# Kernel optimization log

Hardware: AMD Instinct MI355X
Metric: run time of the kernel (lower is better)

## Reference

```python
import jax, jax.numpy as jnp
import numpy as np

B, L, H, D = 2, 1024, 8, 64
DIM = H * D


def setup_inputs() -> dict:
    key = jax.random.key(0)
    ks = jax.random.split(key, 12)
    s = 0.02  # weight init scale
    return {
        "x": jax.random.normal(ks[0], (B, L, DIM), dtype=jnp.float32),
        "wq_w": jax.random.normal(ks[1], (DIM, DIM), dtype=jnp.float32) * s,
        "wq_b": jax.random.normal(ks[2], (DIM,), dtype=jnp.float32) * s,
        "wk_w": jax.random.normal(ks[3], (DIM, DIM), dtype=jnp.float32) * s,
        "wk_b": jax.random.normal(ks[4], (DIM,), dtype=jnp.float32) * s,
        "wv_w": jax.random.normal(ks[5], (DIM, DIM), dtype=jnp.float32) * s,
        "wv_b": jax.random.normal(ks[6], (DIM,), dtype=jnp.float32) * s,
        "phazor_re": jax.random.normal(ks[7], (H, D), dtype=jnp.float32),
        "phazor_im": jax.random.normal(ks[8], (H, D), dtype=jnp.float32),
        "amplitude": jax.random.normal(ks[9], (H,), dtype=jnp.float32),
        "last_conv_re": jax.random.normal(ks[10], (H, D, D), dtype=jnp.float32),
        "last_conv_im": jax.random.normal(ks[11], (H, D, D), dtype=jnp.float32),
    }


def reference(x, wq_w, wq_b, wk_w, wk_b, wv_w, wv_b,
              phazor_re, phazor_im, amplitude, last_conv_re, last_conv_im):
    b, l, _ = x.shape
    h, d = phazor_re.shape
    cplx = jnp.complex64

    q = (x @ wq_w.T + wq_b).reshape(b, l, h, d)
    k = (x @ wk_w.T + wk_b).reshape(b, l, h, d)
    v = (x @ wv_w.T + wv_b).reshape(b, l, h, d)

    phazor_p = (phazor_re + 1j * phazor_im).astype(cplx)      # (H,D)
    phase = phazor_p / jnp.abs(phazor_p)                      # unit-modulus
    amp = jax.nn.sigmoid(amplitude)                           # (H,)
    phazor = phase * amp[:, None]                             # (H,D)

    t = jnp.arange(l)
    phase_prog = phase[None] ** t[:, None, None]              # (L,H,D)
    phase_prog_inv = phase[None] ** (-t)[:, None, None]       # (L,H,D)
    phazor_prog = phazor[None] ** t[:, None, None]            # (L,H,D)

    # cross-chunk: q_t * phazor^{t+1} contracted with initial state (detached)
    last_conv = (last_conv_re + 1j * last_conv_im).astype(cplx)  # (H,D,D)
    qc = q.astype(cplx) * (phazor_prog * phazor[None])[None]     # (B,L,H,D)
    cross = jnp.einsum('blhd,hde->blhe', qc, last_conv)          # (B,L,H,D)

    # decay mask: amp^(i-j) on the lower triangle
    diff = t[:, None] - t[None, :]
    tril = diff >= 0
    mask = jnp.where(tril[None],
                     amp[:, None, None] ** jnp.where(tril, diff, 0)[None],
                     0.0)                                        # (H,L,L)

    qph = q.astype(cplx) * phase_prog[None]                      # (B,L,H,D)
    kph = k.astype(cplx) * phase_prog_inv[None]                  # (B,L,H,D)
    qk = jnp.einsum('blhd,bmhd->bhlm', qph, kph)                 # (B,H,L,L) complex
    qk_mask = qk * mask[None].astype(cplx)
    inner = jnp.einsum('bhlm,bmhd->blhd', qk_mask, v.astype(cplx))

    out = (inner + cross).real.astype(x.dtype).reshape(b, l, h * d)
    return out
```

## Files before the change

### kernel.cpp

```cpp
#include <hip/hip_runtime.h>
#include <hip/hip_bf16.h>
#include <math.h>

#define L_SEQ 1024
#define DIMSZ 512
#define NH 8
#define ND 64
#define NB 2
#define CHUNK 64
#define NC (L_SEQ / CHUNK)
#define BHTOT (NB * NH)
#define MTOT 2048
#define KEFF 512
#define BM 64
#define BN 128

typedef __attribute__((ext_vector_type(8))) _Float16 f16x8;
typedef __attribute__((ext_vector_type(4))) float f32x4;

#define GLD16(g, l) __builtin_amdgcn_global_load_lds( \
    (const __attribute__((address_space(1))) unsigned int*)(g), \
    (__attribute__((address_space(3))) unsigned int*)(l), 16, 0, 0)

__device__ static inline unsigned short f2h(float f) {
    union { _Float16 h; unsigned short u; } x;
    x.h = (_Float16)f;
    return x.u;
}
__device__ static inline float h2f(unsigned short u) {
    union { unsigned short u; _Float16 h; } x;
    x.u = u;
    return (float)x.h;
}
__device__ static inline unsigned packh2(float a, float b) {
    return (unsigned)f2h(a) | ((unsigned)f2h(b) << 16);
}

__global__ __launch_bounds__(256) void pack_kernel(
    const float* __restrict__ x,
    const float* __restrict__ wq, const float* __restrict__ wk, const float* __restrict__ wv,
    const float* __restrict__ lc_re, const float* __restrict__ lc_im,
    unsigned short* __restrict__ A, unsigned short* __restrict__ Bm,
    unsigned* __restrict__ lcT)
{
    __shared__ unsigned T[64][65];
    const int bid = blockIdx.x;
    const int tid = threadIdx.x;
    if (bid < 1024) {
        const int i = bid * 256 + tid;
        const int n  = i >> 7;
        const int kq = (i & 127) << 2;
        const float4 xv = *(const float4*)(x + (size_t)n * DIMSZ + kq);
        *(ushort4*)(A + (size_t)n * KEFF + kq) =
            make_ushort4(f2h(xv.x), f2h(xv.y), f2h(xv.z), f2h(xv.w));
    } else if (bid < 1792) {
        const int idx = bid - 1024;
        const int which = idx >> 8;
        const float* w = which == 0 ? wq : (which == 1 ? wk : wv);
        const int i = (idx & 255) * 256 + tid;
        const int o  = i >> 7;
        const int kq = (i & 127) << 2;
        const float4 wv4 = *(const float4*)(w + (size_t)o * DIMSZ + kq);
        const int row = (which == 0) ? o
                      : 512 + (which - 1) * 64 + (o >> 6) * 128 + (o & 63);
        *(ushort4*)(Bm + (size_t)row * KEFF + kq) =
            make_ushort4(f2h(wv4.x), f2h(wv4.y), f2h(wv4.z), f2h(wv4.w));
    } else {
        const int h = bid - 1792;
        const int e = tid & 63;
        #pragma unroll
        for (int i = 0; i < 16; ++i) {
            const int d = i*4 + (tid >> 6);
            T[e][d] = packh2(lc_re[h*4096 + d*64 + e], lc_im[h*4096 + d*64 + e]);
        }
        __syncthreads();
        const int d = tid & 63;
        #pragma unroll
        for (int i = 0; i < 16; ++i) {
            const int e2 = i*4 + (tid >> 6);
            lcT[h*4096 + e2*64 + d] = T[e2][d];
        }
    }
}

__global__ __launch_bounds__(256) void gemm_kv_kernel(
    const unsigned short* __restrict__ A, const unsigned short* __restrict__ Bm,
    const float* __restrict__ bq, const float* __restrict__ bk, const float* __restrict__ bv,
    const float* __restrict__ ph_re, const float* __restrict__ ph_im,
    const float* __restrict__ ampl,
    unsigned short* __restrict__ qo, unsigned short* __restrict__ ko,
    unsigned short* __restrict__ vo, unsigned* __restrict__ kvB)
{
    __shared__ __align__(16) char lds[49152];
    const int tid  = threadIdx.x;
    const int lane = tid & 63;
    const int wave = tid >> 6;

    const int bid0 = blockIdx.x;
    const int sw = (bid0 & 7) * 48 + (bid0 >> 3);
    const bool isQ = sw < 128;
    int mtile, brow0, h = 0, panel = 0;
    if (isQ) { panel = sw & 3; mtile = sw >> 2; brow0 = panel * 128; }
    else     { const int r = sw - 128; h = r & 7; mtile = r >> 3; brow0 = 512 + h * 128; }
    const int row0 = mtile * 64;
    const int wr = wave >> 1, wc = wave & 1;

    const int srow = tid >> 3;
    const int sin  = (tid & 7) << 4;
    size_t goffA[2], goffB[4];
    #pragma unroll
    for (int c = 0; c < 2; ++c) {
        const int row = c * 32 + srow;
        const int swz = sin ^ ((row & 7) << 4);
        goffA[c] = (size_t)(row0 + row) * (KEFF * 2) + swz;
    }
    #pragma unroll
    for (int c = 0; c < 4; ++c) {
        const int row = c * 32 + srow;
        const int swz = sin ^ ((row & 7) << 4);
        goffB[c] = (size_t)(brow0 + row) * (KEFF * 2) + swz;
    }
    const int ldst = tid * 16;
    const char* Abyte = (const char*)A;
    const char* Bbyte = (const char*)Bm;

    f32x4 acc[2][4];
    const f32x4 zf = {0.f, 0.f, 0.f, 0.f};
    #pragma unroll
    for (int m = 0; m < 2; ++m)
        #pragma unroll
        for (int n = 0; n < 4; ++n) acc[m][n] = zf;

    auto stage = [&](int buf, int t) {
        char* la = lds + buf * 24576;
        char* lb = la + 8192;
        const size_t kb = (size_t)t * 128;
        #pragma unroll
        for (int c = 0; c < 2; ++c)
            GLD16(Abyte + goffA[c] + kb, la + c * 4096 + ldst);
        #pragma unroll
        for (int c = 0; c < 4; ++c)
            GLD16(Bbyte + goffB[c] + kb, lb + c * 4096 + ldst);
    };

    const int rl = lane & 15;
    const int kg = lane >> 4;
    const int rswz = (rl & 7) << 4;

    auto compute = [&](int buf) {
        const char* la = lds + buf * 24576;
        const char* lb = la + 8192;
        #pragma unroll
        for (int ks = 0; ks < 2; ++ks) {
            f16x8 av[2], bvv[4];
            #pragma unroll
            for (int m = 0; m < 2; ++m) {
                const int row = wr * 32 + m * 16 + rl;
                const int addr = (row * 128 + ks * 64 + kg * 16) ^ rswz;
                av[m] = *(const f16x8*)(la + addr);
            }
            #pragma unroll
            for (int n = 0; n < 4; ++n) {
                const int row = wc * 64 + n * 16 + rl;
                const int addr = (row * 128 + ks * 64 + kg * 16) ^ rswz;
                bvv[n] = *(const f16x8*)(lb + addr);
            }
            #pragma unroll
            for (int m = 0; m < 2; ++m)
                #pragma unroll
                for (int n = 0; n < 4; ++n)
                    acc[m][n] = __builtin_amdgcn_mfma_f32_16x16x32_f16(
                        av[m], bvv[n], acc[m][n], 0, 0, 0);
        }
    };

    stage(0, 0);
    __syncthreads();
    const int NT = KEFF / 64;
    for (int t = 0; t < NT; ++t) {
        if (t + 1 < NT) stage((t + 1) & 1, t + 1);
        compute(t & 1);
        __syncthreads();
    }

    if (isQ) {
        #pragma unroll
        for (int n = 0; n < 4; ++n) {
            const int cabs = panel * 128 + wc * 64 + n * 16 + rl;
            const float bs = bq[cabs];
            #pragma unroll
            for (int m = 0; m < 2; ++m) {
                const int rb = row0 + wr * 32 + m * 16 + kg * 4;
                #pragma unroll
                for (int r = 0; r < 4; ++r)
                    qo[(size_t)(rb + r) * DIMSZ + cabs] = f2h(acc[m][n][r] + bs);
            }
        }
        return;
    }

    _Float16 (*KTR)[72] = (_Float16(*)[72])(lds);
    _Float16 (*KTI)[72] = (_Float16(*)[72])(lds + 9216);
    _Float16 (*VWT)[72] = (_Float16(*)[72])(lds + 18432);

    unsigned short* outp = wc == 0 ? ko : vo;
    _Float16 (*RAW)[72] = wc == 0 ? KTR : VWT;
    #pragma unroll
    for (int n = 0; n < 4; ++n) {
        const int cl = h * 64 + n * 16 + rl;
        const float bs = (wc == 0 ? bk : bv)[cl];
        #pragma unroll
        for (int m = 0; m < 2; ++m) {
            const int jb = wr * 32 + m * 16 + kg * 4;
            #pragma unroll
            for (int r = 0; r < 4; ++r) {
                const float val = acc[m][n][r] + bs;
                outp[(size_t)(row0 + jb + r) * DIMSZ + cl] = f2h(val);
                RAW[n * 16 + rl][jb + r] = (_Float16)val;
            }
        }
    }
    __syncthreads();

    const float amp = 1.0f / (1.0f + expf(-ampl[h]));
    const float la_ = logf(amp);
    const float th = atan2f(ph_im[h*ND + lane], ph_re[h*ND + lane]);
    float sth2, cth2; sincosf(th, &sth2, &cth2);
    const float p0 = (float)(CHUNK - 1 - (wave*16 + 15));
    float ap = expf(la_ * p0);
    float sp, cp; sincosf(th * p0, &sp, &cp);
    #pragma unroll
    for (int jj = 15; jj >= 0; --jj) {
        const int j = wave*16 + jj;
        const float kk = (float)KTR[lane][j];
        const float vv = (float)VWT[lane][j];
        KTR[lane][j] = (_Float16)(kk * cp);
        KTI[lane][j] = (_Float16)(kk * sp);
        VWT[lane][j] = (_Float16)(vv * ap);
        const float ncp = cp*cth2 - sp*sth2;
        sp = cp*sth2 + sp*cth2; cp = ncp;
        ap *= amp;
    }
    __syncthreads();

    const int b = mtile >> 4, c = mtile & 15;
    unsigned* dst = kvB + (size_t)(((b * NH + h) << 4) | c) * (ND * ND);
    #pragma unroll
    for (int i = 0; i < 4; ++i) {
        const int mt = wave, nt = i;
        f32x4 aR = zf, aI = zf;
        #pragma unroll
        for (int ks = 0; ks < 2; ++ks) {
            const f16x8 av = *(const f16x8*)&VWT[mt*16 + rl][ks*32 + kg*8];
            const f16x8 br = *(const f16x8*)&KTR[nt*16 + rl][ks*32 + kg*8];
            const f16x8 bi = *(const f16x8*)&KTI[nt*16 + rl][ks*32 + kg*8];
            aR = __builtin_amdgcn_mfma_f32_16x16x32_f16(av, br, aR, 0, 0, 0);
            aI = __builtin_amdgcn_mfma_f32_16x16x32_f16(av, bi, aI, 0, 0, 0);
        }
        const int d = nt*16 + rl;
        #pragma unroll
        for (int r = 0; r < 4; ++r) {
            const int e = mt*16 + kg*4 + r;
            dst[e*ND + d] = packh2(aR[r], aI[r]);
        }
    }
}

__global__ __launch_bounds__(256) void scan_kernel(
    unsigned* __restrict__ kvB, const unsigned* __restrict__ lcT,
    const float* __restrict__ ph_re, const float* __restrict__ ph_im,
    const float* __restrict__ ampl)
{
    const int gid = blockIdx.x * 256 + threadIdx.x;
    const int bh = gid >> 12;
    const int idx = gid & 4095;
    const int h = bh & 7;
    const int d = idx & 63;

    const float th = atan2f(ph_im[h*ND + d], ph_re[h*ND + d]);
    const float la = -logf(1.0f + expf(-ampl[h]));
    const float ampC = expf(la * (float)CHUNK);
    float s, ct; sincosf(th * (float)CHUNK, &s, &ct);
    const float aCr = ampC * ct, aCi = ampC * s;

    unsigned* base = kvB + (size_t)bh * NC * (ND*ND) + idx;
    unsigned tl[NC];
    #pragma unroll
    for (int cc = 0; cc < NC; ++cc) tl[cc] = base[(size_t)cc * (ND*ND)];

    const unsigned lcp = lcT[h*4096 + idx];
    float Sr = h2f((unsigned short)(lcp & 0xffffu));
    float Si = h2f((unsigned short)(lcp >> 16));
    #pragma unroll
    for (int cc = 0; cc < NC; ++cc) {
        base[(size_t)cc * (ND*ND)] = packh2(Sr, Si);
        const float tr = h2f((unsigned short)(tl[cc] & 0xffffu));
        const float ti = h2f((unsigned short)(tl[cc] >> 16));
        const float nr = aCr*Sr - aCi*Si + tr;
        const float ni = aCr*Si + aCi*Sr + ti;
        Sr = nr; Si = ni;
    }
}

__global__ __launch_bounds__(256) void chunk_out_kernel(
    const unsigned short* __restrict__ q, const unsigned short* __restrict__ k,
    const unsigned short* __restrict__ v, const unsigned* __restrict__ Bst,
    const float* __restrict__ ph_re, const float* __restrict__ ph_im,
    const float* __restrict__ ampl, float* __restrict__ out)
{
    __shared__ __align__(16) _Float16 QhR[32][72], QhI[32][72];
    __shared__ __align__(16) _Float16 KhR[64][72], KhI[64][72];
    __shared__ __align__(16) _Float16 VT[64][72];
    __shared__ __align__(16) _Float16 SA[32][72];
    __shared__ float apw[80];

    const int half = blockIdx.x & 1;
    const int bhc = blockIdx.x >> 1;
    const int c  = bhc & (NC - 1);
    const int bh = bhc >> 4;
    const int b = bh >> 3, h = bh & 7;
    const int tid = threadIdx.x;
    const int lane = tid & 63, w = tid >> 6;
    const int rl = lane & 15, kg = lane >> 4;
    const int mt = w >> 1;

    const float la = -logf(1.0f + expf(-ampl[h]));
    if (tid < 72) apw[tid] = expf(la * (float)tid);
    const float th = atan2f(ph_im[h*ND + lane], ph_re[h*ND + lane]);
    float sth_, cth_; sincosf(th, &sth_, &cth_);

    unsigned breg[16];
    const unsigned* Bb = Bst + (size_t)bhc * (ND*ND);
    #pragma unroll
    for (int ii = 0; ii < 16; ++ii) breg[ii] = Bb[ii*256 + tid];

    {
        const int jbase = half*32 + w*8;
        float sr, cr; sincosf(th * (float)jbase, &sr, &cr);
        #pragma unroll
        for (int jj = 0; jj < 8; ++jj) {
            const int row = w*8 + jj;
            const int jabs = jbase + jj;
            const size_t off = ((size_t)(b*L_SEQ + c*CHUNK + jabs)) * DIMSZ + h*ND + lane;
            const float qq = h2f(q[off]);
            QhR[row][lane] = (_Float16)(qq * cr);
            QhI[row][lane] = (_Float16)(qq * sr);
            const float ncr = cr*cth_ - sr*sth_;
            sr = cr*sth_ + sr*cth_; cr = ncr;
        }
    }
    {
        const int kbase = w*16;
        float skr, ckr; sincosf(th * (float)kbase, &skr, &ckr);
        #pragma unroll
        for (int jj = 0; jj < 16; ++jj) {
            const int j = kbase + jj;
            if (half == 0 && j >= 32) {
                VT[lane][j] = (_Float16)0.f;
            } else {
                const size_t off = ((size_t)(b*L_SEQ + c*CHUNK + j)) * DIMSZ + h*ND + lane;
                const float kk = h2f(k[off]), vv = h2f(v[off]);
                KhR[j][lane] = (_Float16)(kk * ckr);
                KhI[j][lane] = (_Float16)(kk * skr);
                VT[lane][j]  = (_Float16)vv;
            }
            const float nck = ckr*cth_ - skr*sth_;
            skr = ckr*sth_ + skr*cth_; ckr = nck;
        }
    }
    __syncthreads();

    const f32x4 zf = {0.f, 0.f, 0.f, 0.f};
    f32x4 sacc[2] = {zf, zf};
    #pragma unroll
    for (int t = 0; t < 2; ++t) {
        const int nt = (w & 1)*2 + t;
        #pragma unroll
        for (int ks = 0; ks < 2; ++ks) {
            const f16x8 aR = *(const f16x8*)&QhR[mt*16 + rl][ks*32 + kg*8];
            const f16x8 bR = *(const f16x8*)&KhR[nt*16 + rl][ks*32 + kg*8];
            sacc[t] = __builtin_amdgcn_mfma_f32_16x16x32_f16(aR, bR, sacc[t], 0, 0, 0);
            const f16x8 aI = *(const f16x8*)&QhI[mt*16 + rl][ks*32 + kg*8];
            const f16x8 bI = *(const f16x8*)&KhI[nt*16 + rl][ks*32 + kg*8];
            sacc[t] = __builtin_amdgcn_mfma_f32_16x16x32_f16(aI, bI, sacc[t], 0, 0, 0);
        }
    }
    __syncthreads();

    #pragma unroll
    for (int t = 0; t < 2; ++t) {
        const int nt = (w & 1)*2 + t;
        #pragma unroll
        for (int r = 0; r < 4; ++r) {
            const int rowm = mt*16 + kg*4 + r;
            const int jabs = half*32 + rowm;
            const int jp = nt*16 + rl;
            const int delta = jabs - jp;
            const float val = (delta >= 0) ? sacc[t][r] * apw[delta] : 0.0f;
            SA[rowm][jp] = (_Float16)val;
        }
    }
    #pragma unroll
    for (int ii = 0; ii < 16; ++ii) {
        const int e = ii*4 + w;
        const float br = h2f((unsigned short)(breg[ii] & 0xffffu));
        const float bi = h2f((unsigned short)(breg[ii] >> 16));
        KhR[e][lane] = (_Float16)(br*cth_ - bi*sth_);
        KhI[e][lane] = (_Float16)(-(br*sth_ + bi*cth_));
    }
    __syncthreads();

    #pragma unroll
    for (int t = 0; t < 2; ++t) {
        const int nt = (w & 1)*2 + t;
        f32x4 accO = zf, accC = zf;
        #pragma unroll
        for (int ks = 0; ks < 2; ++ks) {
            const f16x8 aS = *(const f16x8*)&SA[mt*16 + rl][ks*32 + kg*8];
            const f16x8 bV = *(const f16x8*)&VT[nt*16 + rl][ks*32 + kg*8];
            accO = __builtin_amdgcn_mfma_f32_16x16x32_f16(aS, bV, accO, 0, 0, 0);
            const f16x8 aR = *(const f16x8*)&QhR[mt*16 + rl][ks*32 + kg*8];
            const f16x8 bBR = *(const f16x8*)&KhR[nt*16 + rl][ks*32 + kg*8];
            accC = __builtin_amdgcn_mfma_f32_16x16x32_f16(aR, bBR, accC, 0, 0, 0);
            const f16x8 aI = *(const f16x8*)&QhI[mt*16 + rl][ks*32 + kg*8];
            const f16x8 bBI = *(const f16x8*)&KhI[nt*16 + rl][ks*32 + kg*8];
            accC = __builtin_amdgcn_mfma_f32_16x16x32_f16(aI, bBI, accC, 0, 0, 0);
        }
        const int e = nt*16 + rl;
        #pragma unroll
        for (int r = 0; r < 4; ++r) {
            const int rowm = mt*16 + kg*4 + r;
            const int jabs = half*32 + rowm;
            const float cs = apw[jabs + 1];
            out[((size_t)(b*L_SEQ + c*CHUNK + jabs)) * DIMSZ + h*ND + e] =
                accO[r] + cs * accC[r];
        }
    }
}

extern "C" void kernel_launch(void* const* d_in, const int* in_sizes, int n_in,
                              void* d_out, int out_size, void* d_ws, size_t ws_size,
                              hipStream_t stream)
{
    const float* x     = (const float*)d_in[0];
    const float* wq_w  = (const float*)d_in[1];
    const float* wq_b  = (const float*)d_in[2];
    const float* wk_w  = (const float*)d_in[3];
    const float* wk_b  = (const float*)d_in[4];
    const float* wv_w  = (const float*)d_in[5];
    const float* wv_b  = (const float*)d_in[6];
    const float* ph_re = (const float*)d_in[7];
    const float* ph_im = (const float*)d_in[8];
    const float* ampl  = (const float*)d_in[9];
    const float* lc_re = (const float*)d_in[10];
    const float* lc_im = (const float*)d_in[11];
    float* out = (float*)d_out;

    char* wsb = (char*)d_ws;
    const size_t MB = 1024 * 1024;
    unsigned short* q = (unsigned short*)(wsb + 0);
    unsigned short* k = (unsigned short*)(wsb + 2 * MB);
    unsigned short* v = (unsigned short*)(wsb + 4 * MB);
    unsigned* kvB = (unsigned*)(wsb + 8 * MB);
    unsigned short* Apk = (unsigned short*)(wsb + 13 * MB);
    unsigned short* Bpk = (unsigned short*)(wsb + 16 * MB);
    unsigned* lcT = (unsigned*)(wsb + 18 * MB);

    pack_kernel<<<1800, 256, 0, stream>>>(
        x, wq_w, wk_w, wv_w, lc_re, lc_im, Apk, Bpk, lcT);
    gemm_kv_kernel<<<384, 256, 0, stream>>>(
        Apk, Bpk, wq_b, wk_b, wv_b, ph_re, ph_im, ampl, q, k, v, kvB);
    scan_kernel<<<256, 256, 0, stream>>>(kvB, lcT, ph_re, ph_im, ampl);
    chunk_out_kernel<<<BHTOT * NC * 2, 256, 0, stream>>>(
        q, k, v, kvB, ph_re, ph_im, ampl, out);
}
```

Before: 38.08 us.

## Merge chunk halves into one 512-thread block and skip upper-triangle QK tiles

The output kernel now runs one 512-thread block per (batch, head, chunk) instead of two 256-thread blocks that each handled half the query rows. K and V are loaded and phase-rotated once per chunk rather than twice. Wave tiles above the diagonal skip their QK MFMAs, because the causal mask zeroes those entries anyway. The trade-off is half as many blocks (256), larger LDS per block, and wave divergence in the masked branch.

```diff
diff --git a/kernel.cpp b/kernel.cpp
--- a/kernel.cpp
+++ b/kernel.cpp
@@ -302,72 +302,55 @@
     }
 }
 
-__global__ __launch_bounds__(256) void chunk_out_kernel(
+__global__ __launch_bounds__(512) void chunk_out_kernel(
     const unsigned short* __restrict__ q, const unsigned short* __restrict__ k,
     const unsigned short* __restrict__ v, const unsigned* __restrict__ Bst,
     const float* __restrict__ ph_re, const float* __restrict__ ph_im,
     const float* __restrict__ ampl, float* __restrict__ out)
 {
-    __shared__ __align__(16) _Float16 QhR[32][72], QhI[32][72];
+    __shared__ __align__(16) _Float16 QhR[64][72], QhI[64][72];
     __shared__ __align__(16) _Float16 KhR[64][72], KhI[64][72];
     __shared__ __align__(16) _Float16 VT[64][72];
-    __shared__ __align__(16) _Float16 SA[32][72];
+    __shared__ __align__(16) _Float16 SA[64][72];
     __shared__ float apw[80];
 
-    const int half = blockIdx.x & 1;
-    const int bhc = blockIdx.x >> 1;
+    const int bhc = blockIdx.x;
     const int c  = bhc & (NC - 1);
     const int bh = bhc >> 4;
     const int b = bh >> 3, h = bh & 7;
     const int tid = threadIdx.x;
     const int lane = tid & 63, w = tid >> 6;
     const int rl = lane & 15, kg = lane >> 4;
-    const int mt = w >> 1;
+    const int rt = w >> 1;
 
     const float la = -logf(1.0f + expf(-ampl[h]));
     if (tid < 72) apw[tid] = expf(la * (float)tid);
     const float th = atan2f(ph_im[h*ND + lane], ph_re[h*ND + lane]);
     float sth_, cth_; sincosf(th, &sth_, &cth_);
 
-    unsigned breg[16];
+    unsigned breg[8];
     const unsigned* Bb = Bst + (size_t)bhc * (ND*ND);
     #pragma unroll
-    for (int ii = 0; ii < 16; ++ii) breg[ii] = Bb[ii*256 + tid];
+    for (int ii = 0; ii < 8; ++ii) breg[ii] = Bb[ii*512 + tid];
 
     {
-        const int jbase = half*32 + w*8;
+        const int jbase = w * 8;
         float sr, cr; sincosf(th * (float)jbase, &sr, &cr);
         #pragma unroll
         for (int jj = 0; jj < 8; ++jj) {
-            const int row = w*8 + jj;
-            const int jabs = jbase + jj;
-            const size_t off = ((size_t)(b*L_SEQ + c*CHUNK + jabs)) * DIMSZ + h*ND + lane;
+            const int j = jbase + jj;
+            const size_t off = ((size_t)(b*L_SEQ + c*CHUNK + j)) * DIMSZ + h*ND + lane;
             const float qq = h2f(q[off]);
-            QhR[row][lane] = (_Float16)(qq * cr);
-            QhI[row][lane] = (_Float16)(qq * sr);
+            const float kk = h2f(k[off]);
+            QhR[j][lane] = (_Float16)(qq * cr);
+            QhI[j][lane] = (_Float16)(qq * sr);
+            KhR[j][lane] = (_Float16)(kk * cr);
+            KhI[j][lane] = (_Float16)(kk * sr);
+            VT[lane][j]  = (_Float16)h2f(v[off]);
             const float ncr = cr*cth_ - sr*sth_;
             sr = cr*sth_ + sr*cth_; cr = ncr;
         }
     }
-    {
-        const int kbase = w*16;
-        float skr, ckr; sincosf(th * (float)kbase, &skr, &ckr);
-        #pragma unroll
-        for (int jj = 0; jj < 16; ++jj) {
-            const int j = kbase + jj;
-            if (half == 0 && j >= 32) {
-                VT[lane][j] = (_Float16)0.f;
-            } else {
-                const size_t off = ((size_t)(b*L_SEQ + c*CHUNK + j)) * DIMSZ + h*ND + lane;
-                const float kk = h2f(k[off]), vv = h2f(v[off]);
-                KhR[j][lane] = (_Float16)(kk * ckr);
-                KhI[j][lane] = (_Float16)(kk * skr);
-                VT[lane][j]  = (_Float16)vv;
-            }
-            const float nck = ckr*cth_ - skr*sth_;
-            skr = ckr*sth_ + skr*cth_; ckr = nck;
-        }
-    }
     __syncthreads();
 
     const f32x4 zf = {0.f, 0.f, 0.f, 0.f};
@@ -375,14 +358,16 @@
     #pragma unroll
     for (int t = 0; t < 2; ++t) {
         const int nt = (w & 1)*2 + t;
-        #pragma unroll
-        for (int ks = 0; ks < 2; ++ks) {
-            const f16x8 aR = *(const f16x8*)&QhR[mt*16 + rl][ks*32 + kg*8];
-            const f16x8 bR = *(const f16x8*)&KhR[nt*16 + rl][ks*32 + kg*8];
-            sacc[t] = __builtin_amdgcn_mfma_f32_16x16x32_f16(aR, bR, sacc[t], 0, 0, 0);
-            const f16x8 aI = *(const f16x8*)&QhI[mt*16 + rl][ks*32 + kg*8];
-            const f16x8 bI = *(const f16x8*)&KhI[nt*16 + rl][ks*32 + kg*8];
-            sacc[t] = __builtin_amdgcn_mfma_f32_16x16x32_f16(aI, bI, sacc[t], 0, 0, 0);
+        if (rt >= nt) {
+            #pragma unroll
+            for (int ks = 0; ks < 2; ++ks) {
+                const f16x8 aR = *(const f16x8*)&QhR[rt*16 + rl][ks*32 + kg*8];
+                const f16x8 bR = *(const f16x8*)&KhR[nt*16 + rl][ks*32 + kg*8];
+                sacc[t] = __builtin_amdgcn_mfma_f32_16x16x32_f16(aR, bR, sacc[t], 0, 0, 0);
+                const f16x8 aI = *(const f16x8*)&QhI[rt*16 + rl][ks*32 + kg*8];
+                const f16x8 bI = *(const f16x8*)&KhI[nt*16 + rl][ks*32 + kg*8];
+                sacc[t] = __builtin_amdgcn_mfma_f32_16x16x32_f16(aI, bI, sacc[t], 0, 0, 0);
+            }
         }
     }
     __syncthreads();
@@ -392,17 +377,16 @@
         const int nt = (w & 1)*2 + t;
         #pragma unroll
         for (int r = 0; r < 4; ++r) {
-            const int rowm = mt*16 + kg*4 + r;
-            const int jabs = half*32 + rowm;
+            const int rowm = rt*16 + kg*4 + r;
             const int jp = nt*16 + rl;
-            const int delta = jabs - jp;
+            const int delta = rowm - jp;
             const float val = (delta >= 0) ? sacc[t][r] * apw[delta] : 0.0f;
             SA[rowm][jp] = (_Float16)val;
         }
     }
     #pragma unroll
-    for (int ii = 0; ii < 16; ++ii) {
-        const int e = ii*4 + w;
+    for (int ii = 0; ii < 8; ++ii) {
+        const int e = ii*8 + w;
         const float br = h2f((unsigned short)(breg[ii] & 0xffffu));
         const float bi = h2f((unsigned short)(breg[ii] >> 16));
         KhR[e][lane] = (_Float16)(br*cth_ - bi*sth_);
@@ -416,23 +400,22 @@
         f32x4 accO = zf, accC = zf;
         #pragma unroll
         for (int ks = 0; ks < 2; ++ks) {
-            const f16x8 aS = *(const f16x8*)&SA[mt*16 + rl][ks*32 + kg*8];
+            const f16x8 aS = *(const f16x8*)&SA[rt*16 + rl][ks*32 + kg*8];
             const f16x8 bV = *(const f16x8*)&VT[nt*16 + rl][ks*32 + kg*8];
             accO = __builtin_amdgcn_mfma_f32_16x16x32_f16(aS, bV, accO, 0, 0, 0);
-            const f16x8 aR = *(const f16x8*)&QhR[mt*16 + rl][ks*32 + kg*8];
+            const f16x8 aR = *(const f16x8*)&QhR[rt*16 + rl][ks*32 + kg*8];
             const f16x8 bBR = *(const f16x8*)&KhR[nt*16 + rl][ks*32 + kg*8];
             accC = __builtin_amdgcn_mfma_f32_16x16x32_f16(aR, bBR, accC, 0, 0, 0);
-            const f16x8 aI = *(const f16x8*)&QhI[mt*16 + rl][ks*32 + kg*8];
+            const f16x8 aI = *(const f16x8*)&QhI[rt*16 + rl][ks*32 + kg*8];
             const f16x8 bBI = *(const f16x8*)&KhI[nt*16 + rl][ks*32 + kg*8];
             accC = __builtin_amdgcn_mfma_f32_16x16x32_f16(aI, bBI, accC, 0, 0, 0);
         }
         const int e = nt*16 + rl;
         #pragma unroll
         for (int r = 0; r < 4; ++r) {
-            const int rowm = mt*16 + kg*4 + r;
-            const int jabs = half*32 + rowm;
-            const float cs = apw[jabs + 1];
-            out[((size_t)(b*L_SEQ + c*CHUNK + jabs)) * DIMSZ + h*ND + e] =
+            const int rowm = rt*16 + kg*4 + r;
+            const float cs = apw[rowm + 1];
+            out[((size_t)(b*L_SEQ + c*CHUNK + rowm)) * DIMSZ + h*ND + e] =
                 accO[r] + cs * accC[r];
         }
     }
@@ -471,6 +454,6 @@
     gemm_kv_kernel<<<384, 256, 0, stream>>>(
         Apk, Bpk, wq_b, wk_b, wv_b, ph_re, ph_im, ampl, q, k, v, kvB);
     scan_kernel<<<256, 256, 0, stream>>>(kvB, lcT, ph_re, ph_im, ampl);
-    chunk_out_kernel<<<BHTOT * NC * 2, 256, 0, stream>>>(
+    chunk_out_kernel<<<BHTOT * NC, 512, 0, stream>>>(
         q, k, v, kvB, ph_re, ph_im, ampl, out);
 }
```

New measurement: 32.28 us. 1.18x faster.
